# Kernel tuning notes

Measured on AMD Instinct MI355X. Metric: run time of the kernel, lower is better.

The kernel has to match this reference:

```python
import jax, jax.numpy as jnp
import numpy as np

EMBED_DIM = 1024
NUM_HEADS = 16
HEAD_DIM = EMBED_DIM // NUM_HEADS
SCALE = HEAD_DIM ** -0.5


def setup_inputs() -> dict:
    key = jax.random.key(0)
    ks = jax.random.split(key, 7)
    B, S, D = 4, 2048, EMBED_DIM
    return {
        "x": jax.random.normal(ks[0], (B, S, D), dtype=jnp.float32),
        "gamma": jnp.ones((D,), dtype=jnp.float32),
        "beta": jnp.zeros((D,), dtype=jnp.float32),
        "w_qkv": jax.random.normal(ks[1], (D, 3 * D), dtype=jnp.float32) * (D ** -0.5),
        "b_qkv": jax.random.normal(ks[2], (3 * D,), dtype=jnp.float32) * 0.02,
        "w_proj": jax.random.normal(ks[3], (D, D), dtype=jnp.float32) * (D ** -0.5),
        "b_proj": jax.random.normal(ks[4], (D,), dtype=jnp.float32) * 0.02,
    }


def reference(x, gamma, beta, w_qkv, b_qkv, w_proj, b_proj):
    B, S, D = x.shape
    # pre-norm LayerNorm (eps=1e-5, torch default)
    mu = jnp.mean(x, axis=-1, keepdims=True)
    var = jnp.mean(jnp.square(x - mu), axis=-1, keepdims=True)
    xn = (x - mu) * jax.lax.rsqrt(var + 1e-5) * gamma + beta
    # fused QKV projection -> (3, B, H, S, hd)
    qkv = (xn @ w_qkv + b_qkv).reshape(B, S, 3, NUM_HEADS, HEAD_DIM)
    qkv = jnp.transpose(qkv, (2, 0, 3, 1, 4))
    q, k, v = qkv[0], qkv[1], qkv[2]
    scores = jnp.einsum("bhqd,bhkd->bhqk", q, k) * SCALE
    attn = jax.nn.softmax(scores, axis=-1)  # dropout p=0 -> no-op
    ctx = jnp.einsum("bhqk,bhkd->bhqd", attn, v)
    ctx = jnp.transpose(ctx, (0, 2, 1, 3)).reshape(B, S, D)
    return ctx @ w_proj + b_proj
```

## Files before the change

kernel.cpp:

```cpp
#include <hip/hip_runtime.h>

typedef unsigned short ushort_t;
typedef __attribute__((ext_vector_type(8))) short bf16x8;
typedef __attribute__((ext_vector_type(4))) float f32x4;
typedef __attribute__((ext_vector_type(16))) float f32x16;
typedef __attribute__((ext_vector_type(2))) __bf16 bf16v2;

#define BN 4
#define SEQ 2048
#define DIM 1024
#define NH 16
#define HDIM 64
#define MROWS (BN*SEQ)
#define QSCALE 0.18033688011112042f

__device__ __forceinline__ float bf2f(ushort_t s){ return __uint_as_float(((unsigned)s) << 16); }
__device__ __forceinline__ ushort_t f2bf(float f){
  unsigned u = __float_as_uint(f);
  u += 0x7fffu + ((u >> 16) & 1u);
  return (ushort_t)(u >> 16);
}
__device__ __forceinline__ unsigned pack2(float a, float b){
  return (unsigned)f2bf(a) | ((unsigned)f2bf(b) << 16);
}

__global__ __launch_bounds__(256) void ln_kernel(const float* __restrict__ x,
                                                 const float* __restrict__ gamma,
                                                 const float* __restrict__ beta,
                                                 ushort_t* __restrict__ xnb)
{
  int row = blockIdx.x;
  int t = threadIdx.x;
  float4 v = ((const float4*)(x + (size_t)row * DIM))[t];
  float s = v.x+v.y+v.z+v.w;
  float ss = v.x*v.x+v.y*v.y+v.z*v.z+v.w*v.w;
  #pragma unroll
  for (int o = 32; o > 0; o >>= 1){ s += __shfl_down(s, o); ss += __shfl_down(ss, o); }
  __shared__ float red[10];
  int wid = t >> 6;
  if ((t & 63) == 0){ red[wid] = s; red[4+wid] = ss; }
  __syncthreads();
  if (t == 0){
    float S0 = red[0]+red[1]+red[2]+red[3];
    float SS = red[4]+red[5]+red[6]+red[7];
    float mu = S0 * (1.f/DIM);
    float var = SS * (1.f/DIM) - mu*mu;
    red[8] = mu; red[9] = rsqrtf(var + 1e-5f);
  }
  __syncthreads();
  float mu = red[8], rstd = red[9];
  float4 g = ((const float4*)gamma)[t];
  float4 b = ((const float4*)beta)[t];
  float f0 = (v.x - mu)*rstd*g.x + b.x;
  float f1 = (v.y - mu)*rstd*g.y + b.y;
  float f2 = (v.z - mu)*rstd*g.z + b.z;
  float f3 = (v.w - mu)*rstd*g.w + b.w;
  *(uint2*)(xnb + (size_t)row*DIM + t*4) = make_uint2(pack2(f0,f1), pack2(f2,f3));
}

__global__ __launch_bounds__(256) void cvt_t(const float* __restrict__ src,
                                             ushort_t* __restrict__ dst,
                                             int K, int N, float qscale)
{
  __shared__ float tile[64][65];
  int k0 = blockIdx.y*64, n0 = blockIdx.x*64;
  float sc = (n0 < 1024) ? qscale : 1.f;
  int t = threadIdx.x;
  int c = (t & 15) * 4, r = t >> 4;
  #pragma unroll
  for (int p = 0; p < 4; p++){
    float4 v = *(const float4*)(src + (size_t)(k0 + r + p*16)*N + n0 + c);
    tile[r+p*16][c]   = v.x; tile[r+p*16][c+1] = v.y;
    tile[r+p*16][c+2] = v.z; tile[r+p*16][c+3] = v.w;
  }
  __syncthreads();
  #pragma unroll
  for (int p = 0; p < 4; p++){
    int nn = r + p*16;
    ushort4 o;
    o.x = f2bf(tile[c+0][nn]*sc); o.y = f2bf(tile[c+1][nn]*sc);
    o.z = f2bf(tile[c+2][nn]*sc); o.w = f2bf(tile[c+3][nn]*sc);
    *(ushort4*)(dst + (size_t)(n0+nn)*K + k0 + c) = o;
  }
}

__global__ __launch_bounds__(256) void vtrans(const ushort_t* __restrict__ V,
                                              ushort_t* __restrict__ vt)
{
  __shared__ ushort_t tile[64][72];
  int bh = blockIdx.x >> 5, sc = blockIdx.x & 31;
  int t = threadIdx.x;
  const ushort_t* src = V + ((size_t)bh*SEQ + sc*64)*HDIM;
  #pragma unroll
  for (int p = 0; p < 2; p++){
    int idx = p*256 + t;
    int r = idx >> 3, c8 = (idx & 7)*8;
    *(uint4*)&tile[r][c8] = *(const uint4*)(src + (size_t)r*HDIM + c8);
  }
  __syncthreads();
  ushort_t* dstp = vt + ((size_t)(bh*32 + sc))*HDIM*64;
  #pragma unroll
  for (int p = 0; p < 2; p++){
    int idx = p*256 + t;
    int d = idx >> 3, c8 = (idx & 7)*8;
    uint4 u;
    u.x = (unsigned)tile[c8+0][d] | ((unsigned)tile[c8+1][d] << 16);
    u.y = (unsigned)tile[c8+2][d] | ((unsigned)tile[c8+3][d] << 16);
    u.z = (unsigned)tile[c8+4][d] | ((unsigned)tile[c8+5][d] << 16);
    u.w = (unsigned)tile[c8+6][d] | ((unsigned)tile[c8+7][d] << 16);
    *(uint4*)(dstp + (size_t)d*64 + c8) = u;
  }
}

template<int MODE, int NCOLS>
__global__ __launch_bounds__(256) void mfma_gemm(
    const ushort_t* __restrict__ A,
    const ushort_t* __restrict__ BT,
    const float* __restrict__ bias,
    void* __restrict__ Cv)
{
  __shared__ __align__(16) unsigned char smem[17408];
  ushort_t (*As)[128][8] = (ushort_t(*)[128][8])smem;
  ushort_t (*Bs)[128][8] = (ushort_t(*)[128][8])(smem + 8192);

  int t = threadIdx.x;
  int lane = t & 63, w = t >> 6;
  int col = lane & 15, quad = lane >> 4;
  int n0 = blockIdx.x * 128, m0 = blockIdx.y * 128;
  int sr = t >> 1, h = t & 1;

  f32x4 acc[4][4];
  #pragma unroll
  for (int i = 0; i < 4; i++)
    #pragma unroll
    for (int j = 0; j < 4; j++) acc[i][j] = (f32x4){0.f,0.f,0.f,0.f};

  int mbase = (w & 1)*64 + col;
  int nbase = (w >> 1)*64 + col;

  for (int k0 = 0; k0 < DIM; k0 += 32){
    const ushort_t* ap = A + (size_t)(m0 + sr)*DIM + k0 + h*16;
    uint4 aa0 = *(const uint4*)ap, aa1 = *(const uint4*)(ap + 8);
    const ushort_t* bp = BT + (size_t)(n0 + sr)*DIM + k0 + h*16;
    uint4 bb0 = *(const uint4*)bp, bb1 = *(const uint4*)(bp + 8);

    __syncthreads();
    *(uint4*)&As[2*h  ][sr][0] = aa0;
    *(uint4*)&As[2*h+1][sr][0] = aa1;
    *(uint4*)&Bs[2*h  ][sr][0] = bb0;
    *(uint4*)&Bs[2*h+1][sr][0] = bb1;
    __syncthreads();

    bf16x8 af[4], bfr[4];
    #pragma unroll
    for (int i = 0; i < 4; i++){
      af[i]  = *(const bf16x8*)&As[quad][mbase + i*16][0];
      bfr[i] = *(const bf16x8*)&Bs[quad][nbase + i*16][0];
    }
    #pragma unroll
    for (int mt = 0; mt < 4; mt++)
      #pragma unroll
      for (int nt = 0; nt < 4; nt++)
        acc[mt][nt] = __builtin_amdgcn_mfma_f32_16x16x32_bf16(af[mt], bfr[nt], acc[mt][nt], 0, 0, 0);
  }

  float bscale = (MODE == 2 && n0 < 1024) ? QSCALE : 1.f;
  float bv[4];
  #pragma unroll
  for (int nt = 0; nt < 4; nt++) bv[nt] = bias[n0 + (w>>1)*64 + nt*16 + col] * bscale;

  if (MODE == 2){
    ushort_t (*Cs)[136] = (ushort_t(*)[136])smem;
    ushort_t* C = (ushort_t*)Cv;
    #pragma unroll
    for (int ph = 0; ph < 2; ph++){
      __syncthreads();
      if ((w & 1) == ph){
        #pragma unroll
        for (int mt = 0; mt < 4; mt++)
          #pragma unroll
          for (int nt = 0; nt < 4; nt++)
            #pragma unroll
            for (int r = 0; r < 4; r++)
              Cs[mt*16 + quad*4 + r][(w>>1)*64 + nt*16 + col] = f2bf(acc[mt][nt][r] + bv[nt]);
      }
      __syncthreads();
      #pragma unroll
      for (int p = 0; p < 4; p++){
        int id = p*256 + t;
        int row = id >> 4, cc = id & 15;
        uint4 u = *(const uint4*)&Cs[row][cc*8];
        int m = m0 + ph*64 + row;
        int n = n0 + cc*8;
        int which = n >> 10, hh = (n >> 6) & 15, d = n & 63;
        int b_ = m >> 11, s_ = m & (SEQ-1);
        *(uint4*)&C[((((size_t)which*BN + b_)*NH + hh)*SEQ + s_)*HDIM + d] = u;
      }
    }
  } else {
    float (*Cf)[132] = (float(*)[132])smem;
    float* C = (float*)Cv;
    #pragma unroll
    for (int ph = 0; ph < 4; ph++){
      __syncthreads();
      if ((w & 1) == (ph >> 1)){
        #pragma unroll
        for (int mi = 0; mi < 2; mi++){
          int mt = (ph & 1)*2 + mi;
          #pragma unroll
          for (int nt = 0; nt < 4; nt++)
            #pragma unroll
            for (int r = 0; r < 4; r++)
              Cf[mi*16 + quad*4 + r][(w>>1)*64 + nt*16 + col] = acc[mt][nt][r] + bv[nt];
        }
      }
      __syncthreads();
      #pragma unroll
      for (int p = 0; p < 4; p++){
        int id = p*256 + t;
        int row = id >> 5, cc = id & 31;
        float4 v = *(const float4*)&Cf[row][cc*4];
        int m = m0 + ph*32 + row;
        *(float4*)(C + (size_t)m*NCOLS + n0 + cc*4) = v;
      }
    }
  }
}

__global__ __launch_bounds__(512) void attn_kernel(const ushort_t* __restrict__ qkv,
                                                   const ushort_t* __restrict__ vtp,
                                                   ushort_t* __restrict__ ctx)
{
  __shared__ __align__(16) unsigned char lds[53248];
  ushort_t* Ksm = (ushort_t*)lds;
  ushort_t* Vsm = (ushort_t*)(lds + 8192);

  int t = threadIdx.x;
  int lane = t & 63, w = t >> 6;
  int m32 = lane & 31, half = lane >> 5;
  int r7 = m32 & 7;
  int id = blockIdx.x;
  int bh = (id & 7) | ((id >> 6) << 3);
  int qb = (id >> 3) & 7;

  const size_t PL = (size_t)BN * NH * SEQ * HDIM;
  const ushort_t* Qg = qkv + (size_t)bh * (SEQ * HDIM);
  const ushort_t* Kg = Qg + PL;
  const ushort_t* Vt = vtp + (size_t)bh * 32 * (HDIM * 64);
  int qbase = qb*256 + w*32;

  bf16x8 qf[4];
  #pragma unroll
  for (int c = 0; c < 4; c++)
    qf[c] = *(const bf16x8*)(Qg + (size_t)(qbase + m32)*HDIM + c*16 + half*8);

  bf16x8 ones;
  #pragma unroll
  for (int i = 0; i < 8; i++) ones[i] = (short)0x3F80;

  f32x16 accO[2], accL;
  #pragma unroll
  for (int i = 0; i < 2; i++)
    #pragma unroll
    for (int r = 0; r < 16; r++) accO[i][r] = 0.f;
  #pragma unroll
  for (int r = 0; r < 16; r++) accL[r] = 0.f;

  int srow = t >> 3, och = t & 7;
  const ushort_t* kp0 = Kg + (size_t)srow*HDIM + och*8;
  const ushort_t* vp0 = Vt + (size_t)srow*64 + och*8;
  int wofs = srow*64 + ((och ^ (srow & 7)) << 3);

  uint4 kr = *(const uint4*)kp0;
  uint4 vr = *(const uint4*)vp0;

  for (int kt = 0; kt < 32; kt++){
    __syncthreads();
    *(uint4*)&Ksm[wofs] = kr;
    *(uint4*)&Vsm[wofs] = vr;
    __syncthreads();

    if (kt < 31){
      kr = *(const uint4*)(kp0 + (size_t)(kt+1)*64*HDIM);
      vr = *(const uint4*)(vp0 + (size_t)(kt+1)*HDIM*64);
    }

    bf16x8 pb[4];
    #pragma unroll
    for (int mt = 0; mt < 2; mt++){
      f32x16 z;
      #pragma unroll
      for (int r = 0; r < 16; r++) z[r] = 0.f;
      int rowb = (mt*32 + m32) * 64;
      #pragma unroll
      for (int c = 0; c < 4; c++){
        bf16x8 af = *(const bf16x8*)&Ksm[rowb + (((2*c + half) ^ r7) << 3)];
        z = __builtin_amdgcn_mfma_f32_32x32x16_bf16(af, qf[c], z, 0, 0, 0);
      }
      unsigned u[8];
      #pragma unroll
      for (int i = 0; i < 8; i++){
        float p0 = __builtin_amdgcn_exp2f(z[2*i]);
        float p1 = __builtin_amdgcn_exp2f(z[2*i+1]);
        bf16v2 hh; hh.x = (__bf16)p0; hh.y = (__bf16)p1;
        u[i] = __builtin_bit_cast(unsigned, hh);
      }
      #pragma unroll
      for (int cc = 0; cc < 2; cc++){
        union { uint4 q; bf16x8 b; } cvt;
        cvt.q = make_uint4(u[4*cc+0], u[4*cc+1], u[4*cc+2], u[4*cc+3]);
        pb[mt*2 + cc] = cvt.b;
      }
    }

    #pragma unroll
    for (int kc = 0; kc < 4; kc++){
      accL = __builtin_amdgcn_mfma_f32_32x32x16_bf16(ones, pb[kc], accL, 0, 0, 0);
      #pragma unroll
      for (int md = 0; md < 2; md++){
        int dd = md*32 + m32;
        int rowb = dd * 64;
        union { bf16x8 v8; uint2 u2[2]; } vv;
        vv.u2[0] = *(const uint2*)&Vsm[rowb + (((2*kc  ) ^ r7) << 3) + 4*half];
        vv.u2[1] = *(const uint2*)&Vsm[rowb + (((2*kc+1) ^ r7) << 3) + 4*half];
        accO[md] = __builtin_amdgcn_mfma_f32_32x32x16_bf16(vv.v8, pb[kc], accO[md], 0, 0, 0);
      }
    }
  }

  float inv = 1.f / accL[0];

  ushort_t (*Os)[72] = (ushort_t(*)[72])(lds + 16384 + w*4608);
  #pragma unroll
  for (int md = 0; md < 2; md++)
    #pragma unroll
    for (int g = 0; g < 4; g++){
      int d0 = 8*g + 4*half + 32*md;
      unsigned lo = pack2(accO[md][4*g+0]*inv, accO[md][4*g+1]*inv);
      unsigned hi = pack2(accO[md][4*g+2]*inv, accO[md][4*g+3]*inv);
      *(uint2*)&Os[m32][d0] = make_uint2(lo, hi);
    }

  int b_ = bh >> 4, h_ = bh & 15;
  #pragma unroll
  for (int k = 0; k < 4; k++){
    int row = k*8 + (lane >> 3);
    uint4 u = *(const uint4*)&Os[row][(lane & 7)*8];
    *(uint4*)(ctx + ((size_t)(b_*SEQ + qb*256 + w*32 + row))*DIM + h_*HDIM + (lane & 7)*8) = u;
  }
}

extern "C" void kernel_launch(void* const* d_in, const int* in_sizes, int n_in,
                              void* d_out, int out_size, void* d_ws, size_t ws_size,
                              hipStream_t stream)
{
  const float* x      = (const float*)d_in[0];
  const float* gamma  = (const float*)d_in[1];
  const float* beta   = (const float*)d_in[2];
  const float* w_qkv  = (const float*)d_in[3];
  const float* b_qkv  = (const float*)d_in[4];
  const float* w_proj = (const float*)d_in[5];
  const float* b_proj = (const float*)d_in[6];

  char* ws = (char*)d_ws;
  ushort_t* wqkvT  = (ushort_t*)ws;
  ushort_t* vt     = (ushort_t*)ws;
  ushort_t* wprojT = (ushort_t*)ws;
  ushort_t* qkv    = (ushort_t*)(ws + 16u*1024*1024);
  ushort_t* Vplane = (ushort_t*)(ws + 48u*1024*1024);
  ushort_t* ctx    = (ushort_t*)(ws + 48u*1024*1024);
  ushort_t* xnb    = (ushort_t*)d_out;

  ln_kernel<<<MROWS, 256, 0, stream>>>(x, gamma, beta, xnb);
  cvt_t<<<dim3(3*DIM/64, DIM/64), 256, 0, stream>>>(w_qkv, wqkvT, DIM, 3*DIM, QSCALE);
  mfma_gemm<2, 3*DIM><<<dim3(3*DIM/128, MROWS/128), 256, 0, stream>>>(
      xnb, wqkvT, b_qkv, qkv);
  vtrans<<<BN*NH*(SEQ/64), 256, 0, stream>>>(Vplane, vt);
  attn_kernel<<<BN*NH*(SEQ/256), 512, 0, stream>>>(qkv, vt, ctx);
  cvt_t<<<dim3(DIM/64, DIM/64), 256, 0, stream>>>(w_proj, wprojT, DIM, DIM, 1.f);
  mfma_gemm<0, DIM><<<dim3(DIM/128, MROWS/128), 256, 0, stream>>>(
      ctx, wprojT, b_proj, d_out);
}
```

Measured before the change: 313.7 us.

## Load GEMM tiles directly into LDS with global_load_lds and XOR swizzle

```diff
diff --git a/kernel.cpp b/kernel.cpp
--- a/kernel.cpp
+++ b/kernel.cpp
@@ -23,6 +23,10 @@
 __device__ __forceinline__ unsigned pack2(float a, float b){
   return (unsigned)f2bf(a) | ((unsigned)f2bf(b) << 16);
 }
+
+#define GLL16(gp, lp) __builtin_amdgcn_global_load_lds( \
+    (const __attribute__((address_space(1))) void*)(gp), \
+    (__attribute__((address_space(3))) void*)(lp), 16, 0, 0)
 
 __global__ __launch_bounds__(256) void ln_kernel(const float* __restrict__ x,
                                                  const float* __restrict__ gamma,
@@ -120,14 +124,13 @@
     void* __restrict__ Cv)
 {
   __shared__ __align__(16) unsigned char smem[17408];
-  ushort_t (*As)[128][8] = (ushort_t(*)[128][8])smem;
-  ushort_t (*Bs)[128][8] = (ushort_t(*)[128][8])(smem + 8192);
+  ushort_t* AsL = (ushort_t*)smem;
+  ushort_t* BsL = (ushort_t*)(smem + 8192);
 
   int t = threadIdx.x;
   int lane = t & 63, w = t >> 6;
   int col = lane & 15, quad = lane >> 4;
   int n0 = blockIdx.x * 128, m0 = blockIdx.y * 128;
-  int sr = t >> 1, h = t & 1;
 
   f32x4 acc[4][4];
   #pragma unroll
@@ -138,24 +141,34 @@
   int mbase = (w & 1)*64 + col;
   int nbase = (w >> 1)*64 + col;
 
+  int r0 = (2*w  )*16 + (lane >> 2);
+  int r1 = (2*w+1)*16 + (lane >> 2);
+  int c0 = (((lane & 3) ^ ((r0 & 3) ^ ((r0 >> 2) & 3))) << 3);
+  int c1 = (((lane & 3) ^ ((r1 & 3) ^ ((r1 >> 2) & 3))) << 3);
+  const ushort_t* gA0 = A  + (size_t)(m0 + r0)*DIM + c0;
+  const ushort_t* gA1 = A  + (size_t)(m0 + r1)*DIM + c1;
+  const ushort_t* gB0 = BT + (size_t)(n0 + r0)*DIM + c0;
+  const ushort_t* gB1 = BT + (size_t)(n0 + r1)*DIM + c1;
+  unsigned char* lA0 = smem        + (2*w  )*1024;
+  unsigned char* lA1 = smem        + (2*w+1)*1024;
+  unsigned char* lB0 = smem + 8192 + (2*w  )*1024;
+  unsigned char* lB1 = smem + 8192 + (2*w+1)*1024;
+
+  int ppos = ((quad ^ ((col & 3) ^ ((col >> 2) & 3))) << 3);
+
   for (int k0 = 0; k0 < DIM; k0 += 32){
-    const ushort_t* ap = A + (size_t)(m0 + sr)*DIM + k0 + h*16;
-    uint4 aa0 = *(const uint4*)ap, aa1 = *(const uint4*)(ap + 8);
-    const ushort_t* bp = BT + (size_t)(n0 + sr)*DIM + k0 + h*16;
-    uint4 bb0 = *(const uint4*)bp, bb1 = *(const uint4*)(bp + 8);
-
     __syncthreads();
-    *(uint4*)&As[2*h  ][sr][0] = aa0;
-    *(uint4*)&As[2*h+1][sr][0] = aa1;
-    *(uint4*)&Bs[2*h  ][sr][0] = bb0;
-    *(uint4*)&Bs[2*h+1][sr][0] = bb1;
+    GLL16(gA0 + k0, lA0);
+    GLL16(gA1 + k0, lA1);
+    GLL16(gB0 + k0, lB0);
+    GLL16(gB1 + k0, lB1);
     __syncthreads();
 
     bf16x8 af[4], bfr[4];
     #pragma unroll
     for (int i = 0; i < 4; i++){
-      af[i]  = *(const bf16x8*)&As[quad][mbase + i*16][0];
-      bfr[i] = *(const bf16x8*)&Bs[quad][nbase + i*16][0];
+      af[i]  = *(const bf16x8*)&AsL[(mbase + i*16)*32 + ppos];
+      bfr[i] = *(const bf16x8*)&BsL[(nbase + i*16)*32 + ppos];
     }
     #pragma unroll
     for (int mt = 0; mt < 4; mt++)
```

Measured after the change: 305.1 us. -2.7%, faster.
